# Kernel optimization log

Hardware: AMD Instinct MI355X
Metric: run time of the kernel (lower is better)

The kernel has to match this reference:

```python
import jax, jax.numpy as jnp
import numpy as np

B, S, H, K, V = 1024, 50, 128, 4, 100000
ROUTING_TIMES = 3

def _squash(c):
    # c: [B,K,1,H]
    cap_norm = jnp.sum(jnp.square(c), -1, keepdims=True)
    scalar_factor = cap_norm / (1.0 + cap_norm) / jnp.sqrt(cap_norm + 1e-9)
    return scalar_factor * c

def setup_inputs() -> dict:
    key = jax.random.key(0)
    k1, k2, k3, k4, k5, k6 = jax.random.split(key, 6)
    item_seq = jax.random.randint(k1, (B, S), 0, V)
    mask = jax.random.randint(k2, (B, S), 0, 2).astype(jnp.float32)
    item = jax.random.randint(k3, (B, 1), 0, V)
    emb = jax.random.normal(k4, (V, H), dtype=jnp.float32) * 0.02
    W = jax.random.normal(k5, (H, H), dtype=jnp.float32) * (1.0 / np.sqrt(H))
    # bilinear_type==0 -> capsule routing logits initialized with randn
    capsule_weight0 = jax.random.normal(k6, (B, K, S), dtype=jnp.float32)
    return {"item_seq": item_seq, "mask": mask, "item": item,
            "emb": emb, "W": W, "capsule_weight0": capsule_weight0}

def reference(item_seq, mask, item, emb, W, capsule_weight0):
    # padding_idx=0: lookups see a zeroed row 0 (and get no grad there),
    # but calculate_loss uses the raw weight matrix.
    emb_lookup = emb.at[0].set(0.0)
    seq_emb = emb_lookup[item_seq]          # [B,S,H]
    item_e = emb_lookup[item[:, 0]]         # [B,H]  (squeeze(1))

    # CapsuleNetwork, bilinear_type==0: Linear(H,H,no bias) then repeat_interleave along hidden
    h = seq_emb @ W.T                        # [B,S,H]
    hat = jnp.repeat(h, K, axis=2)           # [B,S,H*K] (repeat_interleave semantics)
    hat = hat.reshape(B, S, K, H).transpose(0, 2, 1, 3)  # [B,K,S,H]
    hat_iter = jax.lax.stop_gradient(hat)    # stop_grad=True (detach)

    atten_mask = jnp.broadcast_to(mask[:, None, :], (B, K, S))
    cw = capsule_weight0
    cap = None
    for i in range(ROUTING_TIMES):
        # torch F.softmax with no dim on a 3-D tensor uses dim=0 (batch axis) -- faithful
        sw = jax.nn.softmax(cw, axis=0)
        sw = jnp.where(atten_mask == 0, 0.0, sw)[:, :, None, :]  # [B,K,1,S]
        src = hat_iter if i < ROUTING_TIMES - 1 else hat
        cap = _squash(sw @ src)                                   # [B,K,1,H]
        if i < ROUTING_TIMES - 1:
            delta = (hat_iter @ jnp.swapaxes(cap, 3, 2)).reshape(B, K, S)
            cw = cw + delta

    user_emb = cap.reshape(B, K, H)          # multi_interest_emb

    # hard readout: pick interest with max dot against target item
    cos = jnp.einsum('bkh,bh->bk', user_emb, item_e)
    k_index = jnp.argmax(cos, axis=1)        # [B]
    best = jnp.take_along_axis(user_emb, k_index[:, None, None], axis=1)[:, 0]  # [B,H]

    # cross-entropy over all items (raw embedding weight)
    scores = best @ emb.T                    # [B,V]
    logp = jax.nn.log_softmax(scores, axis=-1)
    loss = -jnp.mean(jnp.take_along_axis(logp, item, axis=1))
    return user_emb, loss
```

## Files before the change

### kernel.cpp

```cpp
#include <hip/hip_runtime.h>
#include <math.h>

#define BB 1024
#define SS 50
#define SSP 51
#define HH 128
#define KK 4
#define VV 100000
#define NVT 782
#define NVT8 784
#define VPAD (NVT8*128)
#define KS (KK*SS)
#define NHM 400
#define NPAD_ALL 352.0f
#define CONVB 2048
#define LOG2E 1.44269504f
#define SGRID ((NVT8/2)*8)

typedef __attribute__((ext_vector_type(8))) short bf16x8;
typedef __attribute__((ext_vector_type(4))) float f32x4;

__device__ __forceinline__ ushort f2bf(float x) {
  unsigned u = __float_as_uint(x);
  unsigned r = u + 0x7FFF + ((u >> 16) & 1);
  return (ushort)(r >> 16);
}
__device__ __forceinline__ float bf2f(ushort u) {
  return __uint_as_float(((unsigned)u) << 16);
}
__device__ __forceinline__ bf16x8 cvt8(float4 a, float4 b) {
  bf16x8 r;
  r[0] = (short)f2bf(a.x); r[1] = (short)f2bf(a.y);
  r[2] = (short)f2bf(a.z); r[3] = (short)f2bf(a.w);
  r[4] = (short)f2bf(b.x); r[5] = (short)f2bf(b.y);
  r[6] = (short)f2bf(b.z); r[7] = (short)f2bf(b.w);
  return r;
}

__global__ __launch_bounds__(256) void k_pre(const float* __restrict__ emb,
                                             const float* __restrict__ cw0,
                                             float* __restrict__ cm,
                                             float* __restrict__ s1,
                                             float* __restrict__ s2,
                                             float* __restrict__ accum,
                                             const int* __restrict__ item_seq,
                                             const float* __restrict__ W,
                                             ushort* __restrict__ hb16) {
  const int t = threadIdx.x;
  if (blockIdx.x < NHM) {
    __shared__ __align__(16) ushort sWf[32 * 512];
    const int w = t >> 6;
    const int lane = t & 63;
    const int lr = lane & 15;
    const int lq = lane >> 4;
    const int m0 = blockIdx.x * 128;

#pragma unroll
    for (int it = 0; it < 8; ++it) {
      int pos = t + it * 256;
      int ch = pos >> 6, l = pos & 63;
      int n = (ch & 7) * 16 + (l & 15);
      int k0 = (ch >> 3) * 32 + (l >> 4) * 8;
      float4 a = *(const float4*)&W[n * HH + k0];
      float4 b = *(const float4*)&W[n * HH + k0 + 4];
      *(bf16x8*)&sWf[ch * 512 + l * 8] = cvt8(a, b);
    }

    bf16x8 af[4][2];
#pragma unroll
    for (int vv = 0; vv < 2; ++vv) {
      int m = m0 + w * 32 + vv * 16 + lr;
      int idx = item_seq[m];
#pragma unroll
      for (int ks = 0; ks < 4; ++ks) {
        if (idx != 0) {
          float4 a = *(const float4*)&emb[(size_t)idx * HH + ks * 32 + lq * 8];
          float4 b = *(const float4*)&emb[(size_t)idx * HH + ks * 32 + lq * 8 + 4];
          af[ks][vv] = cvt8(a, b);
        } else {
          af[ks][vv] = (bf16x8){0, 0, 0, 0, 0, 0, 0, 0};
        }
      }
    }
    __syncthreads();

    f32x4 acc[8][2];
#pragma unroll
    for (int nt = 0; nt < 8; ++nt)
#pragma unroll
      for (int vv = 0; vv < 2; ++vv) acc[nt][vv] = (f32x4){0.f, 0.f, 0.f, 0.f};

#pragma unroll
    for (int ks = 0; ks < 4; ++ks) {
      bf16x8 bw[8];
#pragma unroll
      for (int nt = 0; nt < 8; ++nt)
        bw[nt] = *(const bf16x8*)&sWf[(ks * 8 + nt) * 512 + lane * 8];
#pragma unroll
      for (int nt = 0; nt < 8; ++nt)
#pragma unroll
        for (int vv = 0; vv < 2; ++vv)
          acc[nt][vv] = __builtin_amdgcn_mfma_f32_16x16x32_bf16(af[ks][vv], bw[nt], acc[nt][vv], 0, 0, 0);
    }

#pragma unroll
    for (int nt = 0; nt < 8; ++nt)
#pragma unroll
      for (int vv = 0; vv < 2; ++vv)
#pragma unroll
        for (int r = 0; r < 4; ++r) {
          int m = m0 + w * 32 + vv * 16 + lq * 4 + r;
          hb16[(size_t)m * HH + nt * 16 + lr] = f2bf(acc[nt][vv][r]);
        }
  } else {
    __shared__ float red[256];
    const int c = blockIdx.x - NHM;
    if (t < 8) s1[t * KS + c] = 0.f;
    if (t >= 8 && t < 16) s2[(t - 8) * KS + c] = 0.f;
    if (c < 32) accum[c * 256 + t] = 0.f;
    float s = 0.f;
    for (int b = t; b < BB; b += 256) s += __expf(cw0[(size_t)b * KS + c]);
    red[t] = s;
    __syncthreads();
    for (int o = 128; o > 0; o >>= 1) {
      if (t < o) red[t] += red[t + o];
      __syncthreads();
    }
    if (t == 0) cm[c] = red[0];
  }
}

__global__ __launch_bounds__(256) void k_route(const float* __restrict__ cwsrc,
                                               float* __restrict__ cwdst,
                                               const ushort* __restrict__ hb16,
                                               const float* __restrict__ csum,
                                               int nslots,
                                               const float* __restrict__ mask,
                                               int last,
                                               float* __restrict__ out_ue,
                                               const float* __restrict__ emb,
                                               const int* __restrict__ item,
                                               ushort* __restrict__ bestb,
                                               float* __restrict__ csnext,
                                               float* __restrict__ si,
                                               ushort* __restrict__ embb) {
  const int t = threadIdx.x;
  if (blockIdx.x >= BB) {
    const size_t stride = (size_t)CONVB * 256 * 4;
    for (size_t i = ((size_t)(blockIdx.x - BB) * 256 + t) * 4;
         i < (size_t)VPAD * HH; i += stride) {
      ushort4 o;
      if (i < (size_t)VV * HH) {
        float4 v = *(const float4*)&emb[i];
        o = make_ushort4(f2bf(v.x), f2bf(v.y), f2bf(v.z), f2bf(v.w));
      } else {
        o = make_ushort4(0, 0, 0, 0);
      }
      *(ushort4*)&embb[i] = o;
    }
    return;
  }

  __shared__ ushort shT[128 * SSP];
  __shared__ float swl[KS];
  __shared__ float c32p[256];
  __shared__ float c32[128];
  __shared__ float csq[128];
  __shared__ float ie4r[32];
  __shared__ float ie4z[32];
  __shared__ float fac[4];
  __shared__ float cosk[4];
  __shared__ float cosr[4];
  __shared__ int kb;
  const int b = blockIdx.x;

  for (int p = t; p < (SS * HH) / 4; p += 256) {
    int flat = 4 * p;
    int s = flat >> 7, col = flat & 127;
    ushort4 v = *(const ushort4*)&hb16[(size_t)b * SS * HH + flat];
    shT[(col + 0) * SSP + s] = v.x;
    shT[(col + 1) * SSP + s] = v.y;
    shT[(col + 2) * SSP + s] = v.z;
    shT[(col + 3) * SSP + s] = v.w;
  }
  if (t < KS) {
    float den = 0.f;
    for (int g2 = 0; g2 < nslots; ++g2) den += csum[g2 * KS + t];
    float v = __expf(cwsrc[(size_t)b * KS + t]) / den;
    if (mask[b * SS + (t % SS)] == 0.0f) v = 0.0f;
    swl[t] = v;
  }
  __syncthreads();

  {
    int col = t & 127;
    int half = t >> 7;
    int k = col >> 5;
    float acc = 0.f;
    const float* swk = &swl[k * SS + half * 25];
    const ushort* hc = &shT[col * SSP + half * 25];
    for (int s = 0; s < 25; ++s) acc += swk[s] * bf2f(hc[s]);
    c32p[t] = acc;
  }
  __syncthreads();
  if (t < 128) c32[t] = c32p[t] + c32p[t + 128];
  __syncthreads();
  if (t < 4) {
    float nrm = 0.f;
#pragma unroll
    for (int j = 0; j < 32; ++j) { float c = c32[32 * t + j]; nrm += c * c; }
    nrm *= 4.0f;
    fac[t] = nrm / (1.0f + nrm) / sqrtf(nrm + 1e-9f);
  }
  __syncthreads();
  if (t < 128) csq[t] = c32[t] * fac[t >> 5];
  __syncthreads();

  if (!last) {
    if (t < KS) {
      int k = t / SS, s = t % SS;
      const float* cq = &csq[32 * k];
      float d = 0.f;
#pragma unroll
      for (int j = 0; j < 32; ++j) d += bf2f(shT[(32 * k + j) * SSP + s]) * cq[j];
      float nv = cwsrc[(size_t)b * KS + t] + 4.0f * d;
      cwdst[(size_t)b * KS + t] = nv;
      atomicAdd(&csnext[(b & 7) * KS + t], __expf(nv));
    }
  } else {
    for (int hh = t; hh < 512; hh += 256) {
      int k = hh >> 7, r = (hh & 127) >> 2;
      out_ue[(size_t)b * 512 + hh] = csq[32 * k + r];
    }
    if (t < 32) {
      int idx = item[b];
      const float* e = emb + (size_t)idx * HH + 4 * t;
      float v = e[0] + e[1] + e[2] + e[3];
      ie4r[t] = v;
      ie4z[t] = (idx == 0) ? 0.f : v;
    }
    __syncthreads();
    if (t < 4) {
      float cz = 0.f, cr = 0.f;
#pragma unroll
      for (int j = 0; j < 32; ++j) {
        cz += csq[32 * t + j] * ie4z[j];
        cr += csq[32 * t + j] * ie4r[j];
      }
      cosk[t] = cz; cosr[t] = cr;
    }
    __syncthreads();
    if (t == 0) {
      int kbest = 0; float bv = cosk[0];
#pragma unroll
      for (int k = 1; k < 4; ++k) if (cosk[k] > bv) { bv = cosk[k]; kbest = k; }
      kb = kbest;
      si[b] = cosr[kbest];
    }
    __syncthreads();
    if (t < 128) bestb[(size_t)b * HH + t] = f2bf(csq[32 * kb + (t >> 2)] * LOG2E);
  }
}

__global__ __launch_bounds__(512) void k_score_mfma(const ushort* __restrict__ bestb,
                                                    const ushort* __restrict__ embb,
                                                    float* __restrict__ accum) {
  const int lin = blockIdx.x;
  const int xcd = lin & 7;
  const int g = lin >> 3;
  const int bt8 = g & 7;
  const int vt0 = xcd * 98 + (g >> 3) * 2;

  __shared__ __align__(16) ushort sB[32 * 512];
  __shared__ float ssm[128][8];
  const int t = threadIdx.x;
  const int w = t >> 6;
  const int lane = t & 63;
  const int lr = lane & 15;
  const int lq = lane >> 4;
  const int b0 = bt8 * 128;
  const int tile = w >> 2;
  const int ws = w & 3;
  const int v0 = (vt0 + tile) * 128 + ws * 32;

  bf16x8 af[4][2];
#pragma unroll
  for (int ks = 0; ks < 4; ++ks)
#pragma unroll
    for (int vv = 0; vv < 2; ++vv)
      af[ks][vv] = *(const bf16x8*)&embb[(size_t)(v0 + vv * 16 + lr) * HH + ks * 32 + lq * 8];

#pragma unroll
  for (int it = 0; it < 4; ++it) {
    int ch = w + it * 8;
    int ks = ch >> 3, bt = ch & 7;
    const ushort* src = &bestb[(size_t)(b0 + bt * 16 + lr) * HH + ks * 32 + lq * 8];
    __builtin_amdgcn_global_load_lds(
        (const __attribute__((address_space(1))) unsigned int*)src,
        (__attribute__((address_space(3))) unsigned int*)&sB[ch * 512 + lane * 8],
        16, 0, 0);
  }

  f32x4 acc[8][2];
#pragma unroll
  for (int bt = 0; bt < 8; ++bt)
#pragma unroll
    for (int vv = 0; vv < 2; ++vv) acc[bt][vv] = (f32x4){0.f, 0.f, 0.f, 0.f};

  __syncthreads();

  bf16x8 bcur[8];
#pragma unroll
  for (int bt = 0; bt < 8; ++bt)
    bcur[bt] = *(const bf16x8*)&sB[bt * 512 + lane * 8];

#pragma unroll
  for (int ks = 0; ks < 4; ++ks) {
    bf16x8 bnxt[8];
    if (ks < 3) {
#pragma unroll
      for (int bt = 0; bt < 8; ++bt)
        bnxt[bt] = *(const bf16x8*)&sB[((ks + 1) * 8 + bt) * 512 + lane * 8];
    }
#pragma unroll
    for (int bt = 0; bt < 8; ++bt)
#pragma unroll
      for (int vv = 0; vv < 2; ++vv)
        acc[bt][vv] = __builtin_amdgcn_mfma_f32_16x16x32_bf16(af[ks][vv], bcur[bt], acc[bt][vv], 0, 0, 0);
    if (ks < 3) {
#pragma unroll
      for (int bt = 0; bt < 8; ++bt) bcur[bt] = bnxt[bt];
    }
  }

#pragma unroll
  for (int bt = 0; bt < 8; ++bt) {
    float e[8];
#pragma unroll
    for (int vv = 0; vv < 2; ++vv)
#pragma unroll
      for (int r = 0; r < 4; ++r)
        e[vv * 4 + r] = __builtin_amdgcn_exp2f(acc[bt][vv][r]);
#pragma unroll
    for (int o = 4; o > 0; o >>= 1)
#pragma unroll
      for (int j = 0; j < 8; ++j)
        if (j < o) e[j] += e[j + o];
    float s = e[0];
    s += __shfl_xor(s, 16);
    s += __shfl_xor(s, 32);
    if (lq == 0) ssm[bt * 16 + lr][w] = s;
  }
  __syncthreads();
  if (t < 128) {
    float s = 0.f;
#pragma unroll
    for (int r = 0; r < 8; ++r) s += ssm[t][r];
    atomicAdd(&accum[(size_t)(lin & 7) * BB + b0 + t], s);
  }
}

__global__ __launch_bounds__(256) void k_loss(const float* __restrict__ accum,
                                              const float* __restrict__ si,
                                              float* __restrict__ outloss) {
  __shared__ float red[256];
  const int t = threadIdx.x;
  float s = 0.f;
  for (int b = t; b < BB; b += 256) {
    float a = 0.f;
#pragma unroll
    for (int r = 0; r < 8; ++r) a += accum[(size_t)r * BB + b];
    s += logf(a - NPAD_ALL) - si[b];
  }
  red[t] = s;
  __syncthreads();
  for (int o = 128; o > 0; o >>= 1) {
    if (t < o) red[t] += red[t + o];
    __syncthreads();
  }
  if (t == 0) outloss[0] = red[0] / (float)BB;
}

extern "C" void kernel_launch(void* const* d_in, const int* in_sizes, int n_in,
                              void* d_out, int out_size, void* d_ws, size_t ws_size,
                              hipStream_t stream) {
  const int*   item_seq = (const int*)d_in[0];
  const float* mask     = (const float*)d_in[1];
  const int*   item     = (const int*)d_in[2];
  const float* emb      = (const float*)d_in[3];
  const float* W        = (const float*)d_in[4];
  const float* cw0      = (const float*)d_in[5];
  float* out = (float*)d_out;
  float* outloss = out + (size_t)BB * KK * HH;

  float* ws = (float*)d_ws;
  float* cm    = ws;
  float* s1    = cm + 256;
  float* s2    = s1 + 8 * KS;
  float* si    = s2 + 8 * KS;
  float* accum = si + BB;
  float* cw    = accum + 8 * BB;
  ushort* hb16  = (ushort*)(cw + (size_t)BB * KS);
  ushort* embb  = hb16 + (size_t)BB * SS * HH;
  ushort* bestb = embb + (size_t)VPAD * HH;

  k_pre<<<dim3(NHM + KS), 256, 0, stream>>>(emb, cw0, cm, s1, s2, accum,
                                            item_seq, W, hb16);

  k_route<<<dim3(BB + CONVB), 256, 0, stream>>>(cw0, cw, hb16, cm, 1, mask, 0, out, emb, item, bestb, s1, si, embb);
  k_route<<<dim3(BB), 256, 0, stream>>>(cw, cw, hb16, s1, 8, mask, 0, out, emb, item, bestb, s2, si, embb);
  k_route<<<dim3(BB), 256, 0, stream>>>(cw, cw, hb16, s2, 8, mask, 1, out, emb, item, bestb, s1, si, embb);

  k_score_mfma<<<dim3(SGRID), 512, 0, stream>>>(bestb, embb, accum);
  k_loss<<<dim3(1), 256, 0, stream>>>(accum, si, outloss);
}
```

Before: 189.4 us.

## Split first two routing iterations into per-(batch,capsule) blocks

Adds a routing kernel that launches one block per (batch, interest) pair instead of one per batch row for the first two routing iterations. Each block loads only its 32-column slice of the bf16 hidden states and computes the weighted sum, squash and logit update for that capsule. This raises parallelism and cuts per-block shared memory. The cost is four times as many small blocks and a partial-sum reduction. The embedding bf16 conversion moves into the new kernel's tail blocks, and the original kernel is kept only for the final iteration.

```diff
diff --git a/kernel.cpp b/kernel.cpp
--- a/kernel.cpp
+++ b/kernel.cpp
@@ -130,6 +130,93 @@
   }
 }
 
+__global__ __launch_bounds__(256) void k_route_bk(const float* __restrict__ cwsrc,
+                                                  float* __restrict__ cwdst,
+                                                  const ushort* __restrict__ hb16,
+                                                  const float* __restrict__ csum,
+                                                  int nslots,
+                                                  const float* __restrict__ mask,
+                                                  const float* __restrict__ emb,
+                                                  ushort* __restrict__ embb,
+                                                  float* __restrict__ csnext) {
+  const int t = threadIdx.x;
+  if (blockIdx.x >= BB * KK) {
+    const size_t stride = (size_t)CONVB * 256 * 4;
+    for (size_t i = ((size_t)(blockIdx.x - BB * KK) * 256 + t) * 4;
+         i < (size_t)VPAD * HH; i += stride) {
+      ushort4 o;
+      if (i < (size_t)VV * HH) {
+        float4 v = *(const float4*)&emb[i];
+        o = make_ushort4(f2bf(v.x), f2bf(v.y), f2bf(v.z), f2bf(v.w));
+      } else {
+        o = make_ushort4(0, 0, 0, 0);
+      }
+      *(ushort4*)&embb[i] = o;
+    }
+    return;
+  }
+
+  const int b = blockIdx.x >> 2;
+  const int k = blockIdx.x & 3;
+
+  __shared__ ushort shT[32 * SSP];
+  __shared__ float swl[SS];
+  __shared__ float c32p[32 * 8];
+  __shared__ float csq[32];
+
+  if (t < 200) {
+    int s = t >> 2, q = t & 3;
+    bf16x8 v = *(const bf16x8*)&hb16[(size_t)b * SS * HH + s * HH + k * 32 + q * 8];
+#pragma unroll
+    for (int i = 0; i < 8; ++i)
+      shT[(q * 8 + i) * SSP + s] = (ushort)v[i];
+  }
+  if (t < SS) {
+    const int c = k * SS + t;
+    float den = 0.f;
+    for (int g2 = 0; g2 < nslots; ++g2) den += csum[g2 * KS + c];
+    float v = __expf(cwsrc[(size_t)b * KS + c]) / den;
+    if (mask[b * SS + t] == 0.0f) v = 0.0f;
+    swl[t] = v;
+  }
+  __syncthreads();
+
+  {
+    int j = t >> 3, h8 = t & 7;
+    float acc = 0.f;
+    const ushort* hc = &shT[j * SSP];
+    for (int s = h8; s < SS; s += 8) acc += swl[s] * bf2f(hc[s]);
+    c32p[t] = acc;
+  }
+  __syncthreads();
+
+  if (t < 32) {
+    float c = 0.f;
+#pragma unroll
+    for (int h8 = 0; h8 < 8; ++h8) c += c32p[t * 8 + h8];
+    float q = c * c;
+    q += __shfl_xor(q, 1);
+    q += __shfl_xor(q, 2);
+    q += __shfl_xor(q, 4);
+    q += __shfl_xor(q, 8);
+    q += __shfl_xor(q, 16);
+    float nrm = 4.0f * q;
+    float fac = nrm / (1.0f + nrm) / sqrtf(nrm + 1e-9f);
+    csq[t] = c * fac;
+  }
+  __syncthreads();
+
+  if (t < SS) {
+    const int c = k * SS + t;
+    float d = 0.f;
+#pragma unroll
+    for (int j = 0; j < 32; ++j) d += bf2f(shT[j * SSP + t]) * csq[j];
+    float nv = cwsrc[(size_t)b * KS + c] + 4.0f * d;
+    cwdst[(size_t)b * KS + c] = nv;
+    atomicAdd(&csnext[(b & 7) * KS + c], __expf(nv));
+  }
+}
+
 __global__ __launch_bounds__(256) void k_route(const float* __restrict__ cwsrc,
                                                float* __restrict__ cwdst,
                                                const ushort* __restrict__ hb16,
@@ -145,22 +232,6 @@
                                                float* __restrict__ si,
                                                ushort* __restrict__ embb) {
   const int t = threadIdx.x;
-  if (blockIdx.x >= BB) {
-    const size_t stride = (size_t)CONVB * 256 * 4;
-    for (size_t i = ((size_t)(blockIdx.x - BB) * 256 + t) * 4;
-         i < (size_t)VPAD * HH; i += stride) {
-      ushort4 o;
-      if (i < (size_t)VV * HH) {
-        float4 v = *(const float4*)&emb[i];
-        o = make_ushort4(f2bf(v.x), f2bf(v.y), f2bf(v.z), f2bf(v.w));
-      } else {
-        o = make_ushort4(0, 0, 0, 0);
-      }
-      *(ushort4*)&embb[i] = o;
-    }
-    return;
-  }
-
   __shared__ ushort shT[128 * SSP];
   __shared__ float swl[KS];
   __shared__ float c32p[256];
@@ -407,8 +478,8 @@
   k_pre<<<dim3(NHM + KS), 256, 0, stream>>>(emb, cw0, cm, s1, s2, accum,
                                             item_seq, W, hb16);
 
-  k_route<<<dim3(BB + CONVB), 256, 0, stream>>>(cw0, cw, hb16, cm, 1, mask, 0, out, emb, item, bestb, s1, si, embb);
-  k_route<<<dim3(BB), 256, 0, stream>>>(cw, cw, hb16, s1, 8, mask, 0, out, emb, item, bestb, s2, si, embb);
+  k_route_bk<<<dim3(BB * KK + CONVB), 256, 0, stream>>>(cw0, cw, hb16, cm, 1, mask, emb, embb, s1);
+  k_route_bk<<<dim3(BB * KK), 256, 0, stream>>>(cw, cw, hb16, s1, 8, mask, emb, embb, s2);
   k_route<<<dim3(BB), 256, 0, stream>>>(cw, cw, hb16, s2, 8, mask, 1, out, emb, item, bestb, s1, si, embb);
 
   k_score_mfma<<<dim3(SGRID), 512, 0, stream>>>(bestb, embb, accum);
```

Result: slower. 193.6 us (+2.2%).

## Persist score blocks over seven vocab tiles with double-buffered A fragments

Applied to the files above, without the earlier changes.

The score kernel now uses 256-thread blocks, and each block loops over seven 128-row vocab tiles instead of two. The B (best-interest) tile is staged in LDS once per block and reused across all seven vocab tiles. The next tile's embedding fragments are register-prefetched while MFMA and exp2 run on the current one. Exp-sums accumulate in registers across tiles, which reduces atomics and the grid to 896 blocks. The risk is lower parallelism and extra register pressure from double-buffered fragments.

```diff
diff --git a/kernel.cpp b/kernel.cpp
--- a/kernel.cpp
+++ b/kernel.cpp
@@ -7,7 +7,6 @@
 #define HH 128
 #define KK 4
 #define VV 100000
-#define NVT 782
 #define NVT8 784
 #define VPAD (NVT8*128)
 #define KS (KK*SS)
@@ -15,7 +14,9 @@
 #define NPAD_ALL 352.0f
 #define CONVB 2048
 #define LOG2E 1.44269504f
-#define SGRID ((NVT8/2)*8)
+#define SVPB 7
+#define SNCH 14
+#define SGRID (8*8*SNCH)
 
 typedef __attribute__((ext_vector_type(8))) short bf16x8;
 typedef __attribute__((ext_vector_type(4))) float f32x4;
@@ -262,37 +263,28 @@
   }
 }
 
-__global__ __launch_bounds__(512) void k_score_mfma(const ushort* __restrict__ bestb,
+__global__ __launch_bounds__(256) void k_score_mfma(const ushort* __restrict__ bestb,
                                                     const ushort* __restrict__ embb,
                                                     float* __restrict__ accum) {
   const int lin = blockIdx.x;
   const int xcd = lin & 7;
-  const int g = lin >> 3;
-  const int bt8 = g & 7;
-  const int vt0 = xcd * 98 + (g >> 3) * 2;
+  const int j = lin >> 3;
+  const int bt8 = j & 7;
+  const int chunk = j >> 3;
+  const int vt0 = xcd * 98 + chunk * SVPB;
 
   __shared__ __align__(16) ushort sB[32 * 512];
-  __shared__ float ssm[128][8];
+  __shared__ float ssm[128][4];
   const int t = threadIdx.x;
   const int w = t >> 6;
   const int lane = t & 63;
   const int lr = lane & 15;
   const int lq = lane >> 4;
   const int b0 = bt8 * 128;
-  const int tile = w >> 2;
-  const int ws = w & 3;
-  const int v0 = (vt0 + tile) * 128 + ws * 32;
-
-  bf16x8 af[4][2];
-#pragma unroll
-  for (int ks = 0; ks < 4; ++ks)
-#pragma unroll
-    for (int vv = 0; vv < 2; ++vv)
-      af[ks][vv] = *(const bf16x8*)&embb[(size_t)(v0 + vv * 16 + lr) * HH + ks * 32 + lq * 8];
-
-#pragma unroll
-  for (int it = 0; it < 4; ++it) {
-    int ch = w + it * 8;
+
+#pragma unroll
+  for (int it = 0; it < 8; ++it) {
+    int ch = w + it * 4;
     int ks = ch >> 3, bt = ch & 7;
     const ushort* src = &bestb[(size_t)(b0 + bt * 16 + lr) * HH + ks * 32 + lq * 8];
     __builtin_amdgcn_global_load_lds(
@@ -301,61 +293,84 @@
         16, 0, 0);
   }
 
-  f32x4 acc[8][2];
-#pragma unroll
-  for (int bt = 0; bt < 8; ++bt)
-#pragma unroll
-    for (int vv = 0; vv < 2; ++vv) acc[bt][vv] = (f32x4){0.f, 0.f, 0.f, 0.f};
-
-  __syncthreads();
-
-  bf16x8 bcur[8];
-#pragma unroll
-  for (int bt = 0; bt < 8; ++bt)
-    bcur[bt] = *(const bf16x8*)&sB[bt * 512 + lane * 8];
-
-#pragma unroll
-  for (int ks = 0; ks < 4; ++ks) {
-    bf16x8 bnxt[8];
-    if (ks < 3) {
-#pragma unroll
-      for (int bt = 0; bt < 8; ++bt)
-        bnxt[bt] = *(const bf16x8*)&sB[((ks + 1) * 8 + bt) * 512 + lane * 8];
-    }
-#pragma unroll
-    for (int bt = 0; bt < 8; ++bt)
-#pragma unroll
-      for (int vv = 0; vv < 2; ++vv)
-        acc[bt][vv] = __builtin_amdgcn_mfma_f32_16x16x32_bf16(af[ks][vv], bcur[bt], acc[bt][vv], 0, 0, 0);
-    if (ks < 3) {
-#pragma unroll
-      for (int bt = 0; bt < 8; ++bt) bcur[bt] = bnxt[bt];
-    }
-  }
+  const ushort* abase = &embb[(size_t)(vt0 * 128 + w * 32 + lr) * HH + lq * 8];
+
+  bf16x8 afA[4][2], afB[4][2];
+#pragma unroll
+  for (int ks = 0; ks < 4; ++ks)
+#pragma unroll
+    for (int vv = 0; vv < 2; ++vv)
+      afA[ks][vv] = *(const bf16x8*)&abase[(size_t)vv * 16 * HH + ks * 32];
+
+  float sacc[8];
+#pragma unroll
+  for (int bt = 0; bt < 8; ++bt) sacc[bt] = 0.f;
+
+  __syncthreads();
+
+  auto tile_body = [&](const bf16x8 (&cur)[4][2], bf16x8 (&nxt)[4][2], int i) {
+    if (i + 1 < SVPB) {
+      const ushort* nb = abase + (size_t)(i + 1) * 128 * HH;
+#pragma unroll
+      for (int ks = 0; ks < 4; ++ks)
+#pragma unroll
+        for (int vv = 0; vv < 2; ++vv)
+          nxt[ks][vv] = *(const bf16x8*)&nb[(size_t)vv * 16 * HH + ks * 32];
+    }
+    __builtin_amdgcn_sched_barrier(0);
+#pragma unroll
+    for (int btp = 0; btp < 4; ++btp) {
+      f32x4 acc[2][2];
+#pragma unroll
+      for (int x = 0; x < 2; ++x)
+#pragma unroll
+        for (int vv = 0; vv < 2; ++vv) acc[x][vv] = (f32x4){0.f, 0.f, 0.f, 0.f};
+#pragma unroll
+      for (int ks = 0; ks < 4; ++ks) {
+        bf16x8 bw0 = *(const bf16x8*)&sB[(ks * 8 + btp * 2 + 0) * 512 + lane * 8];
+        bf16x8 bw1 = *(const bf16x8*)&sB[(ks * 8 + btp * 2 + 1) * 512 + lane * 8];
+#pragma unroll
+        for (int vv = 0; vv < 2; ++vv) {
+          acc[0][vv] = __builtin_amdgcn_mfma_f32_16x16x32_bf16(cur[ks][vv], bw0, acc[0][vv], 0, 0, 0);
+          acc[1][vv] = __builtin_amdgcn_mfma_f32_16x16x32_bf16(cur[ks][vv], bw1, acc[1][vv], 0, 0, 0);
+        }
+      }
+#pragma unroll
+      for (int x = 0; x < 2; ++x) {
+        float e[8];
+#pragma unroll
+        for (int vv = 0; vv < 2; ++vv)
+#pragma unroll
+          for (int r = 0; r < 4; ++r)
+            e[vv * 4 + r] = __builtin_amdgcn_exp2f(acc[x][vv][r]);
+#pragma unroll
+        for (int o = 4; o > 0; o >>= 1)
+#pragma unroll
+          for (int q = 0; q < 8; ++q)
+            if (q < o) e[q] += e[q + o];
+        sacc[btp * 2 + x] += e[0];
+      }
+    }
+  };
+
+  tile_body(afA, afB, 0);
+  tile_body(afB, afA, 1);
+  tile_body(afA, afB, 2);
+  tile_body(afB, afA, 3);
+  tile_body(afA, afB, 4);
+  tile_body(afB, afA, 5);
+  tile_body(afA, afB, 6);
 
 #pragma unroll
   for (int bt = 0; bt < 8; ++bt) {
-    float e[8];
-#pragma unroll
-    for (int vv = 0; vv < 2; ++vv)
-#pragma unroll
-      for (int r = 0; r < 4; ++r)
-        e[vv * 4 + r] = __builtin_amdgcn_exp2f(acc[bt][vv][r]);
-#pragma unroll
-    for (int o = 4; o > 0; o >>= 1)
-#pragma unroll
-      for (int j = 0; j < 8; ++j)
-        if (j < o) e[j] += e[j + o];
-    float s = e[0];
+    float s = sacc[bt];
     s += __shfl_xor(s, 16);
     s += __shfl_xor(s, 32);
     if (lq == 0) ssm[bt * 16 + lr][w] = s;
   }
   __syncthreads();
   if (t < 128) {
-    float s = 0.f;
-#pragma unroll
-    for (int r = 0; r < 8; ++r) s += ssm[t][r];
+    float s = ssm[t][0] + ssm[t][1] + ssm[t][2] + ssm[t][3];
     atomicAdd(&accum[(size_t)(lin & 7) * BB + b0 + t], s);
   }
 }
@@ -411,6 +426,6 @@
   k_route<<<dim3(BB), 256, 0, stream>>>(cw, cw, hb16, s1, 8, mask, 0, out, emb, item, bestb, s2, si, embb);
   k_route<<<dim3(BB), 256, 0, stream>>>(cw, cw, hb16, s2, 8, mask, 1, out, emb, item, bestb, s1, si, embb);
 
-  k_score_mfma<<<dim3(SGRID), 512, 0, stream>>>(bestb, embb, accum);
+  k_score_mfma<<<dim3(SGRID), 256, 0, stream>>>(bestb, embb, accum);
   k_loss<<<dim3(1), 256, 0, stream>>>(accum, si, outloss);
 }
```

After: 196.5 us. 3.7% more time.
